# Kernel optimization log

Measured on AMD Instinct MI355X. Metric: run time of the kernel, lower is better.

The kernel has to match this reference:

```python
import jax, jax.numpy as jnp
import numpy as np

INPUT_DIM = 512
OUTPUT_DIM = 128
MAX_DEPTH = 5          # internal nodes at depths 0..4, leaves at depth 5
BATCH = 16384
N_INT = 2**MAX_DEPTH - 1        # 31 internal nodes (heap order: node i children 2i+1, 2i+2)
N_ALL = 2**(MAX_DEPTH + 1) - 1  # 63 nodes total, each owns a leaf vector


def setup_inputs() -> dict:
    key = jax.random.key(0)
    k0, k1, k2, k3, k4 = jax.random.split(key, 5)
    x = jax.random.normal(k0, (BATCH, INPUT_DIM), dtype=jnp.float32)
    lim = 1.0 / np.sqrt(INPUT_DIM)  # torch nn.Linear default init range
    W = jax.random.uniform(k1, (N_INT, 2, INPUT_DIM), jnp.float32, -lim, lim)
    b = jax.random.uniform(k2, (N_INT, 2), jnp.float32, -lim, lim)
    # gamma initialized to [0.5, 0.5] in the module; perturb slightly so it's not degenerate
    gamma = 0.5 + 0.02 * jax.random.normal(k3, (N_INT, 2), dtype=jnp.float32)
    leaf = jax.random.normal(k4, (N_ALL, OUTPUT_DIM), dtype=jnp.float32)
    return {"x": x, "W": W, "b": b, "gamma": gamma, "leaf": leaf}


def reference(x, W, b, gamma, leaf):
    """Level-by-level (bottom-up) vectorized evaluation of the recursive MixNode tree.

    Per internal node n (heap-indexed):
      router = softmax(x @ W[n].T + b[n])                      # soft routing path of route()
      children = left * router[:,0] + right * router[:,1]      # stack + bmm
      g = softmax(gamma[n])
      y = g[0] * children + g[1] * leaf[n]                     # stack + matmul(gamma)
    Pure leaves (depth == max_depth) return leaf broadcast over batch.
    """
    B = x.shape[0]
    # depth-5 pure leaves: heap indices 31..62 -> Y: [B, 32, O]
    Y = jnp.broadcast_to(leaf[N_INT:N_ALL][None], (B, 2**MAX_DEPTH, leaf.shape[-1]))
    for d in range(MAX_DEPTH - 1, -1, -1):
        s, e = 2**d - 1, 2**(d + 1) - 1   # internal nodes at depth d
        logits = jnp.einsum('bi,nji->bnj', x, W[s:e]) + b[s:e]   # [B, 2^d, 2]
        r = jax.nn.softmax(logits, axis=-1)
        left, right = Y[:, 0::2], Y[:, 1::2]                      # children in heap order
        comb = left * r[..., 0:1] + right * r[..., 1:2]           # [B, 2^d, O]
        g = jax.nn.softmax(gamma[s:e], axis=-1)                   # [2^d, 2]
        Y = g[None, :, 0:1] * comb + g[None, :, 1:2] * leaf[s:e][None]
    return Y[:, 0]  # root output [B, O]
```

## Files before the change

### kernel.cpp

```cpp
#include <hip/hip_runtime.h>
#include <cstdint>

#define BATCH   16384
#define INDIM   512
#define OUTDIM  128
#define NINT    31
#define NALL    63
#define BM      64
#define KCHUNK  128
#define NCHUNKS (INDIM / KCHUNK)
#define THREADS 256

typedef __attribute__((ext_vector_type(8))) short s8v;
typedef __attribute__((ext_vector_type(4))) float f4v;

__device__ __forceinline__ unsigned short f2bf(float f) {
    unsigned int u = __builtin_bit_cast(unsigned int, f);
    u = (u + 0x7FFFu + ((u >> 16) & 1u)) >> 16;
    return (unsigned short)u;
}

#define SWZ(r, k) ((k) ^ (((r) & 7) << 3))

__global__ __launch_bounds__(THREADS) void mixnode_kernel(
    const float* __restrict__ x, const float* __restrict__ W,
    const float* __restrict__ bvec, const float* __restrict__ gamma,
    const float* __restrict__ leaf, float* __restrict__ out)
{
    __shared__ __align__(16) unsigned char regionA[32768];
    __shared__ __align__(16) float Lg[BM][68];
    __shared__ float gsm0[NINT], gsm1[NINT];
    __shared__ float bsh[64];

    unsigned short (*xbf)[KCHUNK] = (unsigned short(*)[KCHUNK])regionA;
    unsigned short (*wbf)[KCHUNK] = (unsigned short(*)[KCHUNK])(regionA + 16384);
    unsigned short (*leafT)[64]   = (unsigned short(*)[64])regionA;
    unsigned short (*cbf)[64]     = (unsigned short(*)[64])(regionA + 16384);

    const int t    = threadIdx.x;
    const int lane = t & 63;
    const int wv   = t >> 6;
    const int g    = lane >> 4;
    const int lm   = lane & 15;
    const int row0 = blockIdx.x * BM;

    if (t < NINT) {
        float g0 = gamma[2*t], g1 = gamma[2*t+1];
        float m  = fmaxf(g0, g1);
        float e0 = __expf(g0 - m), e1 = __expf(g1 - m);
        float inv = 1.0f / (e0 + e1);
        gsm0[t] = e0 * inv; gsm1[t] = e1 * inv;
    }
    if (t < 64) bsh[t] = (t < 62) ? bvec[t] : 0.0f;

    f4v acc[4] = {};
    for (int ch = 0; ch < NCHUNKS; ++ch) {
        const int kc = ch * KCHUNK;
        __syncthreads();
        #pragma unroll
        for (int i = 0; i < 8; ++i) {
            int f  = i * THREADS + t;
            int r  = f >> 5;
            int c4 = f & 31;
            int k0 = c4 * 4;
            int p  = SWZ(r, k0);
            float4 xv = *(const float4*)(x + (size_t)(row0 + r) * INDIM + kc + k0);
            *(ushort4*)&xbf[r][p] = make_ushort4(f2bf(xv.x), f2bf(xv.y), f2bf(xv.z), f2bf(xv.w));
            float4 wvv = make_float4(0.f, 0.f, 0.f, 0.f);
            if (r < 62) wvv = *(const float4*)(W + (size_t)r * INDIM + kc + k0);
            *(ushort4*)&wbf[r][p] = make_ushort4(f2bf(wvv.x), f2bf(wvv.y), f2bf(wvv.z), f2bf(wvv.w));
        }
        __syncthreads();
        #pragma unroll
        for (int ks = 0; ks < KCHUNK / 32; ++ks) {
            int k0 = ks * 32 + 8 * g;
            s8v a = *(const s8v*)&xbf[16*wv + lm][SWZ(lm, k0)];
            #pragma unroll
            for (int c = 0; c < 4; ++c) {
                s8v b = *(const s8v*)&wbf[16*c + lm][SWZ(lm, k0)];
                acc[c] = __builtin_amdgcn_mfma_f32_16x16x32_bf16(a, b, acc[c], 0, 0, 0);
            }
        }
    }
    #pragma unroll
    for (int c = 0; c < 4; ++c)
        #pragma unroll
        for (int r = 0; r < 4; ++r)
            Lg[16*wv + 4*g + r][16*c + lm] = acc[c][r];
    __syncthreads();

    if (t < BM) {
        const int row = t;
        float Pp[NALL];
        float cval[64];
        Pp[0] = 1.0f;
        #pragma unroll
        for (int n = 0; n < NINT; ++n) {
            float l0 = Lg[row][2*n]   + bsh[2*n];
            float l1 = Lg[row][2*n+1] + bsh[2*n+1];
            float r1 = 1.0f / (1.0f + __expf(l0 - l1));
            float base = Pp[n] * gsm0[n];
            Pp[2*n+1] = base * (1.0f - r1);
            Pp[2*n+2] = base * r1;
            cval[n] = Pp[n] * gsm1[n];
        }
        #pragma unroll
        for (int n = NINT; n < NALL; ++n) cval[n] = Pp[n];
        cval[63] = 0.0f;
        #pragma unroll
        for (int c2 = 0; c2 < 8; ++c2) {
            int p = SWZ(row, 8*c2);
            unsigned int a0 = (unsigned)f2bf(cval[8*c2+0]) | ((unsigned)f2bf(cval[8*c2+1]) << 16);
            unsigned int a1 = (unsigned)f2bf(cval[8*c2+2]) | ((unsigned)f2bf(cval[8*c2+3]) << 16);
            unsigned int a2 = (unsigned)f2bf(cval[8*c2+4]) | ((unsigned)f2bf(cval[8*c2+5]) << 16);
            unsigned int a3 = (unsigned)f2bf(cval[8*c2+6]) | ((unsigned)f2bf(cval[8*c2+7]) << 16);
            *(uint4*)&cbf[row][p] = make_uint4(a0, a1, a2, a3);
        }
    } else {
        for (int f = t - 64; f < NALL * 32; f += 192) {
            int n  = f >> 5;
            int c4 = f & 31;
            float4 lv = *(const float4*)(leaf + (size_t)n * OUTDIM + c4 * 4);
            int col = c4 * 4;
            leafT[col+0][SWZ(col+0, n)] = f2bf(lv.x);
            leafT[col+1][SWZ(col+1, n)] = f2bf(lv.y);
            leafT[col+2][SWZ(col+2, n)] = f2bf(lv.z);
            leafT[col+3][SWZ(col+3, n)] = f2bf(lv.w);
        }
        int col = t - 64;
        if (col < OUTDIM) leafT[col][SWZ(col, 63)] = 0;
    }
    __syncthreads();

    f4v o[8] = {};
    #pragma unroll
    for (int kw = 0; kw < 2; ++kw) {
        int k0 = kw * 32 + 8 * g;
        s8v a = *(const s8v*)&cbf[16*wv + lm][SWZ(lm, k0)];
        #pragma unroll
        for (int nt = 0; nt < 8; ++nt) {
            s8v b = *(const s8v*)&leafT[16*nt + lm][SWZ(lm, k0)];
            o[nt] = __builtin_amdgcn_mfma_f32_16x16x32_bf16(a, b, o[nt], 0, 0, 0);
        }
    }
    #pragma unroll
    for (int nt = 0; nt < 8; ++nt)
        #pragma unroll
        for (int r = 0; r < 4; ++r)
            out[(size_t)(row0 + 16*wv + 4*g + r) * OUTDIM + 16*nt + lm] = o[nt][r];
}

extern "C" void kernel_launch(void* const* d_in, const int* in_sizes, int n_in,
                              void* d_out, int out_size, void* d_ws, size_t ws_size,
                              hipStream_t stream) {
    const float* x     = (const float*)d_in[0];
    const float* W     = (const float*)d_in[1];
    const float* b     = (const float*)d_in[2];
    const float* gamma = (const float*)d_in[3];
    const float* leaf  = (const float*)d_in[4];
    float* out = (float*)d_out;
    hipLaunchKernelGGL(mixnode_kernel, dim3(BATCH / BM), dim3(THREADS), 0, stream,
                       x, W, b, gamma, leaf, out);
}
```

Measured before the change: 91.92 us.

## Precompute bf16 weights and leaves in prep kernel; stream x directly into MFMA

Adds a small prep kernel that converts W and the transposed leaf table to bf16 and precomputes bias and gamma softmax into the workspace. The main kernel no longer stages x and W through LDS. Each wave loads its x rows straight from global memory, converts them in registers, and reads the bf16 W and leaf fragments directly from global/L2. This removes per-block redundant W and leaf conversion and several barriers. The costs are a second launch, uncoalesced per-lane row reads of x, and reliance on cache for W reuse.

```diff
diff --git a/kernel.cpp b/kernel.cpp
--- a/kernel.cpp
+++ b/kernel.cpp
@@ -1,41 +1,73 @@
 #include <hip/hip_runtime.h>
+#include <hip/hip_bf16.h>
 #include <cstdint>
 
 #define BATCH   16384
 #define INDIM   512
 #define OUTDIM  128
 #define NINT    31
-#define NALL    63
 #define BM      64
-#define KCHUNK  128
-#define NCHUNKS (INDIM / KCHUNK)
 #define THREADS 256
+
+#define WS_WBF    0u
+#define WS_LEAFT  65536u
+#define WS_BIAS   81920u
+#define WS_GSM0   82176u
+#define WS_GSM1   82432u
 
 typedef __attribute__((ext_vector_type(8))) short s8v;
 typedef __attribute__((ext_vector_type(4))) float f4v;
 
-__device__ __forceinline__ unsigned short f2bf(float f) {
-    unsigned int u = __builtin_bit_cast(unsigned int, f);
-    u = (u + 0x7FFFu + ((u >> 16) & 1u)) >> 16;
-    return (unsigned short)u;
+__device__ __forceinline__ short bfs(float f) {
+    return (short)__builtin_bit_cast(unsigned short, __float2bfloat16(f));
+}
+__device__ __forceinline__ unsigned int pk2(float lo, float hi) {
+    return (unsigned int)(unsigned short)bfs(lo) |
+           ((unsigned int)(unsigned short)bfs(hi) << 16);
 }
 
 #define SWZ(r, k) ((k) ^ (((r) & 7) << 3))
 
-__global__ __launch_bounds__(THREADS) void mixnode_kernel(
-    const float* __restrict__ x, const float* __restrict__ W,
-    const float* __restrict__ bvec, const float* __restrict__ gamma,
-    const float* __restrict__ leaf, float* __restrict__ out)
+__global__ __launch_bounds__(256) void prep_kernel(
+    const float* __restrict__ W, const float* __restrict__ bvec,
+    const float* __restrict__ gamma, const float* __restrict__ leaf,
+    unsigned char* __restrict__ ws)
 {
-    __shared__ __align__(16) unsigned char regionA[32768];
-    __shared__ __align__(16) float Lg[BM][68];
-    __shared__ float gsm0[NINT], gsm1[NINT];
-    __shared__ float bsh[64];
+    unsigned short* wbf = (unsigned short*)(ws + WS_WBF);
+    unsigned short* lT  = (unsigned short*)(ws + WS_LEAFT);
+    float* bias = (float*)(ws + WS_BIAS);
+    float* g0v  = (float*)(ws + WS_GSM0);
+    float* g1v  = (float*)(ws + WS_GSM1);
+    const int tid  = blockIdx.x * 256 + threadIdx.x;
+    const int nthr = gridDim.x * 256;
 
-    unsigned short (*xbf)[KCHUNK] = (unsigned short(*)[KCHUNK])regionA;
-    unsigned short (*wbf)[KCHUNK] = (unsigned short(*)[KCHUNK])(regionA + 16384);
-    unsigned short (*leafT)[64]   = (unsigned short(*)[64])regionA;
-    unsigned short (*cbf)[64]     = (unsigned short(*)[64])(regionA + 16384);
+    for (int i = tid; i < 64 * INDIM; i += nthr) {
+        int r = i >> 9;
+        float v = (r < 62) ? W[i] : 0.0f;
+        wbf[i] = (unsigned short)bfs(v);
+    }
+    for (int i = tid; i < OUTDIM * 64; i += nthr) {
+        int n = i & 63, col = i >> 6;
+        float v = (n < 63) ? leaf[(size_t)n * OUTDIM + col] : 0.0f;
+        lT[i] = (unsigned short)bfs(v);
+    }
+    if (tid < 64) bias[tid] = (tid < 62) ? bvec[tid] : 0.0f;
+    if (tid < NINT) {
+        float a = gamma[2*tid], b = gamma[2*tid+1];
+        float m = fmaxf(a, b);
+        float e0 = __expf(a - m), e1 = __expf(b - m);
+        float inv = 1.0f / (e0 + e1);
+        g0v[tid] = e0 * inv;
+        g1v[tid] = e1 * inv;
+    }
+}
+
+__global__ __launch_bounds__(THREADS) void mix_main(
+    const float* __restrict__ x, const unsigned char* __restrict__ ws,
+    float* __restrict__ out)
+{
+    __shared__ __align__(16) float Lg[BM][65];
+    __shared__ __align__(16) unsigned short cbf[BM][64];
 
     const int t    = threadIdx.x;
     const int lane = t & 63;
@@ -44,42 +76,28 @@
     const int lm   = lane & 15;
     const int row0 = blockIdx.x * BM;
 
-    if (t < NINT) {
-        float g0 = gamma[2*t], g1 = gamma[2*t+1];
-        float m  = fmaxf(g0, g1);
-        float e0 = __expf(g0 - m), e1 = __expf(g1 - m);
-        float inv = 1.0f / (e0 + e1);
-        gsm0[t] = e0 * inv; gsm1[t] = e1 * inv;
+    const float* bias = (const float*)(ws + WS_BIAS);
+    f4v acc[4];
+    #pragma unroll
+    for (int c = 0; c < 4; ++c) {
+        float b = bias[16*c + lm];
+        acc[c] = (f4v){b, b, b, b};
     }
-    if (t < 64) bsh[t] = (t < 62) ? bvec[t] : 0.0f;
 
-    f4v acc[4] = {};
-    for (int ch = 0; ch < NCHUNKS; ++ch) {
-        const int kc = ch * KCHUNK;
-        __syncthreads();
+    const float* xrow = x + (size_t)(row0 + 16*wv + lm) * INDIM;
+    const unsigned short* wb = (const unsigned short*)(ws + WS_WBF);
+    #pragma unroll
+    for (int ks = 0; ks < INDIM / 32; ++ks) {
+        const int k0 = ks * 32 + 8 * g;
+        float4 x0 = *(const float4*)(xrow + k0);
+        float4 x1 = *(const float4*)(xrow + k0 + 4);
+        s8v a;
+        a[0] = bfs(x0.x); a[1] = bfs(x0.y); a[2] = bfs(x0.z); a[3] = bfs(x0.w);
+        a[4] = bfs(x1.x); a[5] = bfs(x1.y); a[6] = bfs(x1.z); a[7] = bfs(x1.w);
         #pragma unroll
-        for (int i = 0; i < 8; ++i) {
-            int f  = i * THREADS + t;
-            int r  = f >> 5;
-            int c4 = f & 31;
-            int k0 = c4 * 4;
-            int p  = SWZ(r, k0);
-            float4 xv = *(const float4*)(x + (size_t)(row0 + r) * INDIM + kc + k0);
-            *(ushort4*)&xbf[r][p] = make_ushort4(f2bf(xv.x), f2bf(xv.y), f2bf(xv.z), f2bf(xv.w));
-            float4 wvv = make_float4(0.f, 0.f, 0.f, 0.f);
-            if (r < 62) wvv = *(const float4*)(W + (size_t)r * INDIM + kc + k0);
-            *(ushort4*)&wbf[r][p] = make_ushort4(f2bf(wvv.x), f2bf(wvv.y), f2bf(wvv.z), f2bf(wvv.w));
-        }
-        __syncthreads();
-        #pragma unroll
-        for (int ks = 0; ks < KCHUNK / 32; ++ks) {
-            int k0 = ks * 32 + 8 * g;
-            s8v a = *(const s8v*)&xbf[16*wv + lm][SWZ(lm, k0)];
-            #pragma unroll
-            for (int c = 0; c < 4; ++c) {
-                s8v b = *(const s8v*)&wbf[16*c + lm][SWZ(lm, k0)];
-                acc[c] = __builtin_amdgcn_mfma_f32_16x16x32_bf16(a, b, acc[c], 0, 0, 0);
-            }
+        for (int c = 0; c < 4; ++c) {
+            s8v b = *(const s8v*)(wb + (size_t)(16*c + lm) * INDIM + k0);
+            acc[c] = __builtin_amdgcn_mfma_f32_16x16x32_bf16(a, b, acc[c], 0, 0, 0);
         }
     }
     #pragma unroll
@@ -91,55 +109,43 @@
 
     if (t < BM) {
         const int row = t;
-        float Pp[NALL];
-        float cval[64];
+        const float* g0v = (const float*)(ws + WS_GSM0);
+        const float* g1v = (const float*)(ws + WS_GSM1);
+        float Pp[63];
+        float cv[64];
         Pp[0] = 1.0f;
         #pragma unroll
         for (int n = 0; n < NINT; ++n) {
-            float l0 = Lg[row][2*n]   + bsh[2*n];
-            float l1 = Lg[row][2*n+1] + bsh[2*n+1];
+            float l0 = Lg[row][2*n];
+            float l1 = Lg[row][2*n + 1];
             float r1 = 1.0f / (1.0f + __expf(l0 - l1));
-            float base = Pp[n] * gsm0[n];
-            Pp[2*n+1] = base * (1.0f - r1);
-            Pp[2*n+2] = base * r1;
-            cval[n] = Pp[n] * gsm1[n];
+            float base = Pp[n] * g0v[n];
+            Pp[2*n + 1] = base * (1.0f - r1);
+            Pp[2*n + 2] = base * r1;
+            cv[n] = Pp[n] * g1v[n];
         }
         #pragma unroll
-        for (int n = NINT; n < NALL; ++n) cval[n] = Pp[n];
-        cval[63] = 0.0f;
+        for (int n = NINT; n < 63; ++n) cv[n] = Pp[n];
+        cv[63] = 0.0f;
         #pragma unroll
         for (int c2 = 0; c2 < 8; ++c2) {
-            int p = SWZ(row, 8*c2);
-            unsigned int a0 = (unsigned)f2bf(cval[8*c2+0]) | ((unsigned)f2bf(cval[8*c2+1]) << 16);
-            unsigned int a1 = (unsigned)f2bf(cval[8*c2+2]) | ((unsigned)f2bf(cval[8*c2+3]) << 16);
-            unsigned int a2 = (unsigned)f2bf(cval[8*c2+4]) | ((unsigned)f2bf(cval[8*c2+5]) << 16);
-            unsigned int a3 = (unsigned)f2bf(cval[8*c2+6]) | ((unsigned)f2bf(cval[8*c2+7]) << 16);
-            *(uint4*)&cbf[row][p] = make_uint4(a0, a1, a2, a3);
+            int p = SWZ(row, 8 * c2);
+            *(uint4*)&cbf[row][p] = make_uint4(
+                pk2(cv[8*c2+0], cv[8*c2+1]), pk2(cv[8*c2+2], cv[8*c2+3]),
+                pk2(cv[8*c2+4], cv[8*c2+5]), pk2(cv[8*c2+6], cv[8*c2+7]));
         }
-    } else {
-        for (int f = t - 64; f < NALL * 32; f += 192) {
-            int n  = f >> 5;
-            int c4 = f & 31;
-            float4 lv = *(const float4*)(leaf + (size_t)n * OUTDIM + c4 * 4);
-            int col = c4 * 4;
-            leafT[col+0][SWZ(col+0, n)] = f2bf(lv.x);
-            leafT[col+1][SWZ(col+1, n)] = f2bf(lv.y);
-            leafT[col+2][SWZ(col+2, n)] = f2bf(lv.z);
-            leafT[col+3][SWZ(col+3, n)] = f2bf(lv.w);
-        }
-        int col = t - 64;
-        if (col < OUTDIM) leafT[col][SWZ(col, 63)] = 0;
     }
     __syncthreads();
 
+    const unsigned short* lT = (const unsigned short*)(ws + WS_LEAFT);
     f4v o[8] = {};
     #pragma unroll
     for (int kw = 0; kw < 2; ++kw) {
-        int k0 = kw * 32 + 8 * g;
+        const int k0 = kw * 32 + 8 * g;
         s8v a = *(const s8v*)&cbf[16*wv + lm][SWZ(lm, k0)];
         #pragma unroll
         for (int nt = 0; nt < 8; ++nt) {
-            s8v b = *(const s8v*)&leafT[16*nt + lm][SWZ(lm, k0)];
+            s8v b = *(const s8v*)(lT + (size_t)(16*nt + lm) * 64 + k0);
             o[nt] = __builtin_amdgcn_mfma_f32_16x16x32_bf16(a, b, o[nt], 0, 0, 0);
         }
     }
@@ -159,6 +165,8 @@
     const float* gamma = (const float*)d_in[3];
     const float* leaf  = (const float*)d_in[4];
     float* out = (float*)d_out;
-    hipLaunchKernelGGL(mixnode_kernel, dim3(BATCH / BM), dim3(THREADS), 0, stream,
-                       x, W, b, gamma, leaf, out);
+    hipLaunchKernelGGL(prep_kernel, dim3(64), dim3(256), 0, stream,
+                       W, b, gamma, leaf, (unsigned char*)d_ws);
+    hipLaunchKernelGGL(mix_main, dim3(BATCH / BM), dim3(THREADS), 0, stream,
+                       x, (const unsigned char*)d_ws, out);
 }
```

Result: slower. 95.51 us (+3.9%).
